# Kernel tuning notes

Measured on AMD Instinct MI355X. Metric: run time of the kernel, lower is better.

The kernel has to match this reference:

```python
import jax, jax.numpy as jnp
import numpy as np

D_MODEL = 2048
HEADS = 16
INNER = 8192
SEQ = 2048
BATCH = 1  # source code's mask.reshape(B,1,L,L) requires B==1
EPS = 1e-5


def _layer_norm(x, gamma, beta):
    mu = jnp.mean(x, axis=-1, keepdims=True)
    var = jnp.mean(jnp.square(x - mu), axis=-1, keepdims=True)
    return (x - mu) * jax.lax.rsqrt(var + EPS) * gamma + beta


def setup_inputs() -> dict:
    key = jax.random.key(0)
    ks = jax.random.split(key, 14)
    s = 0.02
    return {
        "x": jax.random.normal(ks[0], (BATCH, SEQ, D_MODEL), jnp.float32),
        # weights stored as (in, out)
        "Wqkv": jax.random.normal(ks[1], (D_MODEL, 3 * D_MODEL), jnp.float32) * s,
        "bqkv": jnp.zeros((3 * D_MODEL,), jnp.float32),
        "Wo": jax.random.normal(ks[2], (D_MODEL, D_MODEL), jnp.float32) * s,
        "bo": jnp.zeros((D_MODEL,), jnp.float32),
        "W1": jax.random.normal(ks[3], (D_MODEL, INNER), jnp.float32) * s,
        "b1": jnp.zeros((INNER,), jnp.float32),
        "W2": jax.random.normal(ks[4], (INNER, D_MODEL), jnp.float32) * s,
        "b2": jnp.zeros((D_MODEL,), jnp.float32),
        "g1": jnp.ones((D_MODEL,), jnp.float32),
        "be1": jnp.zeros((D_MODEL,), jnp.float32),
        "g2": jnp.ones((D_MODEL,), jnp.float32),
        "be2": jnp.zeros((D_MODEL,), jnp.float32),
    }


def reference(x, Wqkv, bqkv, Wo, bo, W1, b1, W2, b2, g1, be1, g2, be2):
    B, L, D = x.shape
    H, hd = HEADS, D // HEADS
    qkv = x @ Wqkv + bqkv                       # [B,L,3D]
    q, k, v = jnp.split(qkv, 3, axis=-1)
    q = q.reshape(B, L, H, hd)
    k = k.reshape(B, L, H, hd)
    v = v.reshape(B, L, H, hd)
    # NOTE: faithful to source, scale is 1/sqrt(D) not 1/sqrt(head_dim)
    scores = jnp.einsum("bqhd,bkhd->bhqk", q, k) / jnp.sqrt(jnp.float32(D))
    causal = jnp.tril(jnp.ones((L, L), bool))   # [L,L] broadcast over B,H
    scores = jnp.where(causal, scores, -jnp.inf)
    attn = jax.nn.softmax(scores, axis=-1)      # dropout = identity (eval)
    out = jnp.einsum("bhqk,bkhd->bqhd", attn, v).reshape(B, L, D)
    lin = out @ Wo + bo
    h = _layer_norm(x + lin, g1, be1)
    ff = jax.nn.gelu(h @ W1 + b1, approximate=False) @ W2 + b2
    return _layer_norm(h + ff, g2, be2)
```

## Files before the change

kernel.cpp:

```cpp
#include <hip/hip_runtime.h>
#include <hip/hip_bf16.h>

typedef unsigned short u16;
typedef __attribute__((ext_vector_type(8))) short frag8;
typedef __attribute__((ext_vector_type(4))) float facc4;

#define L_SEQ 2048
#define D_MODEL 2048
#define N_HEADS 16
#define HEAD_D 128
#define N_QKV 6144
#define D_INNER 8192

__device__ __forceinline__ u16 f2b(float f) {
    __hip_bfloat16 h = __float2bfloat16(f);
    return *reinterpret_cast<u16*>(&h);
}

__device__ __forceinline__ float b2f(u16 u) {
    __hip_bfloat16 h = *reinterpret_cast<__hip_bfloat16*>(&u);
    return __bfloat162float(h);
}

__device__ __forceinline__ void gload_lds16(const void* g, void* l) {
    __builtin_amdgcn_global_load_lds(
        (const __attribute__((address_space(1))) unsigned int*)g,
        (__attribute__((address_space(3))) unsigned int*)l, 16, 0, 0);
}

__device__ __forceinline__ float gelu_exact(float x) {
    return 0.5f * x * (1.0f + erff(x * 0.7071067811865475f));
}

__global__ __launch_bounds__(256) void cvt_bf16_kernel(const float* __restrict__ in, u16* __restrict__ out, int n) {
    const int i = (blockIdx.x * 256 + threadIdx.x) * 8;
    if (i >= n) return;
    float4 a = *(const float4*)(in + i);
    float4 b = *(const float4*)(in + i + 4);
    u16 tmp[8];
    tmp[0] = f2b(a.x); tmp[1] = f2b(a.y); tmp[2] = f2b(a.z); tmp[3] = f2b(a.w);
    tmp[4] = f2b(b.x); tmp[5] = f2b(b.y); tmp[6] = f2b(b.z); tmp[7] = f2b(b.w);
    *(uint4*)(out + i) = *(uint4*)tmp;
}

__global__ __launch_bounds__(256) void tr_cvt64(const float* __restrict__ in, u16* __restrict__ out, int R, int C) {
    __shared__ float t[64][68];
    const int bx = blockIdx.x * 64;
    const int by = blockIdx.y * 64;
    const int tid = threadIdx.x;
    {
        const int r = tid >> 2;
        const int c4 = (tid & 3) * 16;
        const float* src = in + (size_t)(by + r) * C + bx + c4;
#pragma unroll
        for (int j = 0; j < 4; ++j)
            *(float4*)&t[r][c4 + 4 * j] = *(const float4*)(src + 4 * j);
    }
    __syncthreads();
    {
        const int cc = tid >> 2;
        const int rr0 = (tid & 3) * 16;
        u16 tmp[16];
#pragma unroll
        for (int j = 0; j < 16; ++j) tmp[j] = f2b(t[rr0 + j][cc]);
        u16* dst = out + (size_t)(bx + cc) * R + by + rr0;
        *(uint4*)(dst) = *(uint4*)&tmp[0];
        *(uint4*)(dst + 8) = *(uint4*)&tmp[8];
    }
}

template <int EPI>
__global__ __launch_bounds__(512, 2) void gemm256(const u16* __restrict__ A, const u16* __restrict__ Bt,
                                                  const float* __restrict__ bias, void* __restrict__ Cout,
                                                  u16* __restrict__ q0, u16* __restrict__ q1,
                                                  u16* __restrict__ q2, u16* __restrict__ q3,
                                                  int M, int N, int K, int kseg, int nbm) {
    __shared__ u16 lds[2 * 32768];
    const int tid = threadIdx.x;
    const int lane = tid & 63, wid = tid >> 6;
    const int wm = wid >> 2, wn = wid & 3;
    const int l15 = lane & 15, g4 = lane >> 4;

    const int nwg = gridDim.x;
    const int q8 = nwg >> 3;
    const int wg = (blockIdx.x & 7) * q8 + (blockIdx.x >> 3);
    const int bm = wg % nbm, bn = wg / nbm;
    const int kb = blockIdx.z * kseg;
    const int ksz = (blockIdx.z == (int)gridDim.z - 1) ? (K - kb) : kseg;
    const int nt = ksz >> 6;

    const int rr = tid >> 3;
    const int kk8 = tid & 7;
    const int srcE = (kk8 ^ (rr & 7)) << 3;
    const u16* aS = A + (size_t)(bm * 256 + rr) * K + kb + srcE;
    const u16* bS = Bt + (size_t)(bn * 256 + ((rr >> 5) << 6) + (rr & 31)) * K + kb + srcE;
    const size_t r128 = (size_t)128 * K;
    const size_t r64 = (size_t)64 * K;
    const size_t c32 = (size_t)32 * K;

    auto stA = [&](int tt, int h) {
        u16* d = &lds[((tt & 1) << 15) + (h << 13)];
        const u16* g = aS + (size_t)tt * 64 + (h ? r64 : 0);
        gload_lds16(g, d + tid * 8);
        gload_lds16(g + r128, d + 4096 + tid * 8);
    };
    auto stB = [&](int tt, int h) {
        u16* d = &lds[((tt & 1) << 15) + 16384 + (h << 13)];
        const u16* g = bS + (size_t)tt * 64 + (h ? c32 : 0);
        gload_lds16(g, d + tid * 8);
        gload_lds16(g + r128, d + 4096 + tid * 8);
    };

    const int ch0 = (g4 ^ (l15 & 7)) << 3;
    const int ch1 = ch0 ^ 32;
    const int aRdBase = (wm * 64 + l15) * 64;
    const int bRdBase = (wn * 32 + l15) * 64;

    frag8 a[4][2], b0[2][2], b1[2][2];
    facc4 acc[8][4] = {};

    auto rdA = [&](int bufo, int mh) {
#pragma unroll
        for (int mi = 0; mi < 4; ++mi) {
            const int base = bufo + mh * 8192 + aRdBase + mi * 1024;
            a[mi][0] = *(const frag8*)&lds[base + ch0];
            a[mi][1] = *(const frag8*)&lds[base + ch1];
        }
    };
    auto rdB = [&](int bufo, int nh, frag8(&bb)[2][2]) {
#pragma unroll
        for (int ni = 0; ni < 2; ++ni) {
            const int base = bufo + 16384 + nh * 8192 + bRdBase + ni * 1024;
            bb[ni][0] = *(const frag8*)&lds[base + ch0];
            bb[ni][1] = *(const frag8*)&lds[base + ch1];
        }
    };
    auto quad = [&](int mh, int nh, frag8(&bb)[2][2]) {
        __builtin_amdgcn_s_setprio(1);
#pragma unroll
        for (int kh = 0; kh < 2; ++kh)
#pragma unroll
            for (int mi = 0; mi < 4; ++mi)
#pragma unroll
                for (int ni = 0; ni < 2; ++ni)
                    acc[mh * 4 + mi][nh * 2 + ni] =
                        __builtin_amdgcn_mfma_f32_16x16x32_bf16(a[mi][kh], bb[ni][kh],
                                                                acc[mh * 4 + mi][nh * 2 + ni], 0, 0, 0);
        __builtin_amdgcn_s_setprio(0);
    };

#define SB __builtin_amdgcn_sched_barrier(0)
#define BAR __builtin_amdgcn_s_barrier()

    stA(0, 0); stB(0, 0); stB(0, 1); stA(0, 1);
    if (nt > 1) { stA(1, 0); stB(1, 0); stB(1, 1); }
    if (nt > 2) asm volatile("s_waitcnt vmcnt(6)" ::: "memory");
    else        asm volatile("s_waitcnt vmcnt(0)" ::: "memory");
    BAR; SB;

    for (int t = 0; t < nt; ++t) {
        const int bufo = (t & 1) << 15;
        rdA(bufo, 0);
        rdB(bufo, 0, b0);
        if (t + 1 < nt) stA(t + 1, 1);
        SB; BAR; SB;
        quad(0, 0, b0);
        BAR; SB;
        rdB(bufo, 1, b1);
        if (t + 2 < nt) stA(t + 2, 0);
        SB; BAR; SB;
        quad(0, 1, b1);
        BAR; SB;
        rdA(bufo, 1);
        if (t + 2 < nt) stB(t + 2, 0);
        SB; BAR; SB;
        quad(1, 0, b0);
        BAR; SB;
        if (t + 2 < nt) stB(t + 2, 1);
        SB; BAR; SB;
        quad(1, 1, b1);
        if (t + 2 < nt) asm volatile("s_waitcnt vmcnt(6)" ::: "memory");
        else            asm volatile("s_waitcnt vmcnt(0)" ::: "memory");
        BAR; SB;
    }
#undef SB
#undef BAR

    const int row0 = bm * 256 + wm * 128 + g4 * 4;
    const int col0 = bn * 256 + wn * 64 + l15;
    u16* pout = nullptr;
    if (EPI == 3) {
        const int z = blockIdx.z;
        pout = (z == 0) ? q0 : (z == 1) ? q1 : (z == 2) ? q2 : q3;
    }
#pragma unroll
    for (int nf = 0; nf < 4; nf++) {
        const int col = col0 + nf * 16;
        const float bv = (EPI == 3) ? 0.0f : bias[col];
#pragma unroll
        for (int mf = 0; mf < 8; mf++) {
#pragma unroll
            for (int r = 0; r < 4; r++) {
                const int row = row0 + mf * 16 + r;
                float v = acc[mf][nf][r] + bv;
                if (EPI == 2) v = gelu_exact(v);
                if (EPI == 0)
                    ((float*)Cout)[(size_t)row * N + col] = v;
                else if (EPI == 3)
                    pout[(size_t)row * N + col] = f2b(v);
                else
                    ((u16*)Cout)[(size_t)row * N + col] = f2b(v);
            }
        }
    }
}

__global__ __launch_bounds__(256) void attn_kernel(const u16* __restrict__ qkv, u16* __restrict__ out) {
    __shared__ u16 kT[2][64 * 128];
    __shared__ u16 vT[2][128 * 64];
    const int h = blockIdx.y;
    const int qb = (blockIdx.y < 8) ? ((int)gridDim.x - 1 - (int)blockIdx.x) : (int)blockIdx.x;
    const int tid = threadIdx.x;
    const int lane = tid & 63, w = tid >> 6;
    const int l15 = lane & 15, g4 = lane >> 4;
    const int q0 = qb * 64 + w * 16;
    const float scale = 0.022097086912079608f;

    frag8 qf[4];
    {
        const u16* qrow = qkv + (size_t)(q0 + l15) * N_QKV + h * HEAD_D + g4 * 8;
#pragma unroll
        for (int c = 0; c < 4; c++) qf[c] = *(const frag8*)(qrow + c * 32);
    }

    float m_run = -1e30f, l_run = 0.0f;
    facc4 o[8] = {};

    const int src0 = ((g4 & 1) << 5) + l15;
    const int src1 = src0 + 16;
    const bool hi = (g4 & 2) != 0;

    const int nt = qb + 1;

    auto stageK = [&](int kbase, int buf) {
        const u16* kg_ptr = qkv + (size_t)kbase * N_QKV + D_MODEL + h * HEAD_D;
#pragma unroll
        for (int p = 0; p < 4; ++p) {
            const int c = p * 256 + tid;
            const int row = c >> 4;
            const int colb = (c & 15) << 4;
            const int srcb = colb ^ ((row & 7) << 4);
            gload_lds16(kg_ptr + (size_t)row * N_QKV + (srcb >> 1), &kT[buf][c * 8]);
        }
    };
    auto loadV = [&](int kbase, uint4 (&vv)[4]) {
        const u16* vg_ptr = qkv + (size_t)kbase * N_QKV + 2 * D_MODEL + h * HEAD_D;
#pragma unroll
        for (int i = 0; i < 4; ++i)
            vv[i] = *(const uint4*)(vg_ptr + (size_t)lane * N_QKV + w * 32 + i * 8);
    };
    auto writeV = [&](const uint4 (&vv)[4], int buf) {
#pragma unroll
        for (int i = 0; i < 4; ++i) {
            const u16* pv = (const u16*)&vv[i];
#pragma unroll
            for (int e = 0; e < 8; ++e) {
                const int d = w * 32 + i * 8 + e;
                vT[buf][d * 64 + ((((lane >> 3) ^ (d & 7)) << 3) | (lane & 7))] = pv[e];
            }
        }
    };

    {
        uint4 vv[4];
        stageK(0, 0);
        loadV(0, vv);
        writeV(vv, 0);
    }
    __syncthreads();

    for (int t = 0; t < nt; ++t) {
        const int buf = t & 1;
        const int kbase = t * 64;
        const bool last = (t == nt - 1);

        uint4 vv[4];
        if (!last) {
            stageK(kbase + 64, buf ^ 1);
            loadV(kbase + 64, vv);
        }

        const u16* kTb = kT[buf];
        const u16* vTb = vT[buf];
        float st[16];
        float mx = -1e30f;
#pragma unroll
        for (int ks = 0; ks < 4; ++ks) {
            const bool active = !last || (ks <= w);
            if (active) {
                facc4 s = {};
                const int kl = ks * 16 + l15;
#pragma unroll
                for (int c = 0; c < 4; ++c) {
                    const int colb = (g4 * 16 + c * 64) ^ ((kl & 7) << 4);
                    frag8 kf = *(const frag8*)&kTb[kl * 128 + (colb >> 1)];
                    s = __builtin_amdgcn_mfma_f32_16x16x32_bf16(kf, qf[c], s, 0, 0, 0);
                }
#pragma unroll
                for (int r = 0; r < 4; ++r) {
                    float v = s[r] * scale;
                    if (last) {
                        const int key = kbase + ks * 16 + g4 * 4 + r;
                        if (key > q0 + l15) v = -1e30f;
                    }
                    st[ks * 4 + r] = v;
                    mx = fmaxf(mx, v);
                }
            } else {
#pragma unroll
                for (int r = 0; r < 4; ++r) st[ks * 4 + r] = -1e30f;
            }
        }

        mx = fmaxf(mx, __shfl_xor(mx, 16));
        mx = fmaxf(mx, __shfl_xor(mx, 32));
        const bool skip = __all(mx <= m_run + 8.0f);
        const float m_new = skip ? m_run : fmaxf(m_run, mx);
        const float alpha = __expf(m_run - m_new);
        float ps = 0.0f;
        uint2 pb[4];
#pragma unroll
        for (int ks = 0; ks < 4; ++ks) {
            const float p0 = __expf(st[ks * 4 + 0] - m_new);
            const float p1 = __expf(st[ks * 4 + 1] - m_new);
            const float p2 = __expf(st[ks * 4 + 2] - m_new);
            const float p3 = __expf(st[ks * 4 + 3] - m_new);
            ps += (p0 + p1) + (p2 + p3);
            pb[ks].x = (unsigned)f2b(p0) | ((unsigned)f2b(p1) << 16);
            pb[ks].y = (unsigned)f2b(p2) | ((unsigned)f2b(p3) << 16);
        }
        ps += __shfl_xor(ps, 16);
        ps += __shfl_xor(ps, 32);
        l_run = l_run * alpha + ps;
        m_run = m_new;
        if (!skip) {
#pragma unroll
            for (int c8 = 0; c8 < 8; ++c8)
#pragma unroll
                for (int r = 0; r < 4; ++r) o[c8][r] *= alpha;
        }

#pragma unroll
        for (int kp = 0; kp < 2; ++kp) {
            const bool kp_active = !last || (kp == 0) || (w >= 2);
            if (kp_active) {
                const uint2 a = pb[2 * kp], b = pb[2 * kp + 1];
                const unsigned a0 = __shfl(a.x, src0), a1 = __shfl(a.y, src0);
                const unsigned a2 = __shfl(a.x, src1), a3 = __shfl(a.y, src1);
                const unsigned b0 = __shfl(b.x, src0), b1 = __shfl(b.y, src0);
                const unsigned b2 = __shfl(b.x, src1), b3 = __shfl(b.y, src1);
                union { unsigned u[4]; frag8 f; } pu;
                pu.u[0] = hi ? b0 : a0;
                pu.u[1] = hi ? b1 : a1;
                pu.u[2] = hi ? b2 : a2;
                pu.u[3] = hi ? b3 : a3;
                const frag8 pf = pu.f;
#pragma unroll
                for (int c8 = 0; c8 < 8; ++c8) {
                    const int d = c8 * 16 + l15;
                    const int ch = (((kp * 4 + g4) ^ (l15 & 7)) << 3);
                    frag8 vf = *(const frag8*)&vTb[d * 64 + ch];
                    o[c8] = __builtin_amdgcn_mfma_f32_16x16x32_bf16(vf, pf, o[c8], 0, 0, 0);
                }
            }
        }

        if (!last) writeV(vv, buf ^ 1);
        __syncthreads();
    }

    const float inv_l = 1.0f / l_run;
    u16* orow = out + (size_t)(q0 + l15) * D_MODEL + h * HEAD_D;
#pragma unroll
    for (int c8 = 0; c8 < 8; ++c8) {
        uint2 st2;
        st2.x = (unsigned)f2b(o[c8][0] * inv_l) | ((unsigned)f2b(o[c8][1] * inv_l) << 16);
        st2.y = (unsigned)f2b(o[c8][2] * inv_l) | ((unsigned)f2b(o[c8][3] * inv_l) << 16);
        *(uint2*)&orow[c8 * 16 + g4 * 4] = st2;
    }
}

__global__ __launch_bounds__(256) void ln1_part_kernel(const float* __restrict__ x,
                                                       const u16* __restrict__ p0, const u16* __restrict__ p1,
                                                       const u16* __restrict__ p2, const u16* __restrict__ p3,
                                                       const float* __restrict__ bias,
                                                       const float* __restrict__ gamma, const float* __restrict__ beta,
                                                       u16* __restrict__ outb) {
    __shared__ float red[8];
    const int row = blockIdx.x;
    const int tid = threadIdx.x;
    const size_t rb = (size_t)row * D_MODEL;
    float v[8];
    float s = 0.0f, s2 = 0.0f;
#pragma unroll
    for (int i = 0; i < 8; i++) {
        const int c = tid + i * 256;
        float xv = x[rb + c] + bias[c] +
                   b2f(p0[rb + c]) + b2f(p1[rb + c]) + b2f(p2[rb + c]) + b2f(p3[rb + c]);
        v[i] = xv;
        s += xv;
        s2 += xv * xv;
    }
#pragma unroll
    for (int off = 32; off; off >>= 1) {
        s += __shfl_xor(s, off);
        s2 += __shfl_xor(s2, off);
    }
    if ((tid & 63) == 0) { red[(tid >> 6) * 2] = s; red[(tid >> 6) * 2 + 1] = s2; }
    __syncthreads();
    s = red[0] + red[2] + red[4] + red[6];
    s2 = red[1] + red[3] + red[5] + red[7];
    const float mean = s * (1.0f / D_MODEL);
    const float var = s2 * (1.0f / D_MODEL) - mean * mean;
    const float rstd = rsqrtf(var + 1e-5f);
#pragma unroll
    for (int i = 0; i < 8; i++) {
        const int c = tid + i * 256;
        outb[rb + c] = f2b((v[i] - mean) * rstd * gamma[c] + beta[c]);
    }
}

__global__ __launch_bounds__(256) void ln_part_kernel(const u16* __restrict__ hb,
                                                      const u16* __restrict__ p0, const u16* __restrict__ p1,
                                                      const u16* __restrict__ p2, const u16* __restrict__ p3,
                                                      const float* __restrict__ bias,
                                                      const float* __restrict__ gamma, const float* __restrict__ beta,
                                                      float* __restrict__ outf) {
    __shared__ float red[8];
    const int row = blockIdx.x;
    const int tid = threadIdx.x;
    const size_t rb = (size_t)row * D_MODEL;
    float v[8];
    float s = 0.0f, s2 = 0.0f;
#pragma unroll
    for (int i = 0; i < 8; i++) {
        const int c = tid + i * 256;
        float x = b2f(hb[rb + c]) + bias[c] +
                  b2f(p0[rb + c]) + b2f(p1[rb + c]) + b2f(p2[rb + c]) + b2f(p3[rb + c]);
        v[i] = x;
        s += x;
        s2 += x * x;
    }
#pragma unroll
    for (int off = 32; off; off >>= 1) {
        s += __shfl_xor(s, off);
        s2 += __shfl_xor(s2, off);
    }
    if ((tid & 63) == 0) { red[(tid >> 6) * 2] = s; red[(tid >> 6) * 2 + 1] = s2; }
    __syncthreads();
    s = red[0] + red[2] + red[4] + red[6];
    s2 = red[1] + red[3] + red[5] + red[7];
    const float mean = s * (1.0f / D_MODEL);
    const float var = s2 * (1.0f / D_MODEL) - mean * mean;
    const float rstd = rsqrtf(var + 1e-5f);
#pragma unroll
    for (int i = 0; i < 8; i++) {
        const int c = tid + i * 256;
        outf[rb + c] = (v[i] - mean) * rstd * gamma[c] + beta[c];
    }
}

extern "C" void kernel_launch(void* const* d_in, const int* in_sizes, int n_in,
                              void* d_out, int out_size, void* d_ws, size_t ws_size,
                              hipStream_t stream) {
    const float* x    = (const float*)d_in[0];
    const float* Wqkv = (const float*)d_in[1];
    const float* bqkv = (const float*)d_in[2];
    const float* Wo   = (const float*)d_in[3];
    const float* bo   = (const float*)d_in[4];
    const float* W1   = (const float*)d_in[5];
    const float* b1   = (const float*)d_in[6];
    const float* W2   = (const float*)d_in[7];
    const float* b2   = (const float*)d_in[8];
    const float* g1   = (const float*)d_in[9];
    const float* be1  = (const float*)d_in[10];
    const float* g2   = (const float*)d_in[11];
    const float* be2  = (const float*)d_in[12];

    char* ws = (char*)d_ws;
    const size_t MB = 1024 * 1024;
    u16*  xb     = (u16*)(ws + 0);
    u16*  WqkvT  = (u16*)(ws + 8 * MB);
    u16*  qkv    = (u16*)(ws + 32 * MB);
    u16*  attn_o = (u16*)(ws + 56 * MB);
    u16*  WoT    = (u16*)(ws + 8 * MB);
    u16*  pp0    = (u16*)(ws + 16 * MB);
    u16*  pp1    = (u16*)(ws + 24 * MB);
    u16*  pp2    = (u16*)(ws + 32 * MB);
    u16*  pp3    = (u16*)(ws + 40 * MB);
    u16*  hb     = (u16*)(ws + 0);
    u16*  W1T    = (u16*)(ws + 8 * MB);
    u16*  f1     = (u16*)(ws + 40 * MB);
    u16*  W2T    = (u16*)(ws + 72 * MB);
    u16*  part0  = (u16*)(ws + 8 * MB);
    u16*  part1  = (u16*)(ws + 16 * MB);
    u16*  part2  = (u16*)(ws + 24 * MB);
    u16*  part3  = (u16*)(ws + 32 * MB);

    cvt_bf16_kernel<<<2048, 256, 0, stream>>>(x, xb, L_SEQ * D_MODEL);
    tr_cvt64<<<dim3(N_QKV / 64, D_MODEL / 64), 256, 0, stream>>>(Wqkv, WqkvT, D_MODEL, N_QKV);
    gemm256<1><<<dim3(192, 1, 1), 512, 0, stream>>>(xb, WqkvT, bqkv, qkv, nullptr, nullptr, nullptr, nullptr,
                                                    L_SEQ, N_QKV, D_MODEL, D_MODEL, 8);
    attn_kernel<<<dim3(L_SEQ / 64, N_HEADS), 256, 0, stream>>>(qkv, attn_o);
    tr_cvt64<<<dim3(D_MODEL / 64, D_MODEL / 64), 256, 0, stream>>>(Wo, WoT, D_MODEL, D_MODEL);
    gemm256<3><<<dim3(64, 1, 4), 512, 0, stream>>>(attn_o, WoT, nullptr, nullptr, pp0, pp1, pp2, pp3,
                                                   L_SEQ, D_MODEL, D_MODEL, 512, 8);
    ln1_part_kernel<<<L_SEQ, 256, 0, stream>>>(x, pp0, pp1, pp2, pp3, bo, g1, be1, hb);
    tr_cvt64<<<dim3(D_INNER / 64, D_MODEL / 64), 256, 0, stream>>>(W1, W1T, D_MODEL, D_INNER);
    gemm256<2><<<dim3(256, 1, 1), 512, 0, stream>>>(hb, W1T, b1, f1, nullptr, nullptr, nullptr, nullptr,
                                                    L_SEQ, D_INNER, D_MODEL, D_MODEL, 8);
    tr_cvt64<<<dim3(D_MODEL / 64, D_INNER / 64), 256, 0, stream>>>(W2, W2T, D_INNER, D_MODEL);
    gemm256<3><<<dim3(64, 1, 4), 512, 0, stream>>>(f1, W2T, nullptr, nullptr, part0, part1, part2, part3,
                                                   L_SEQ, D_MODEL, D_INNER, 2048, 8);
    ln_part_kernel<<<L_SEQ, 256, 0, stream>>>(hb, part0, part1, part2, part3, b2, g2, be2, (float*)d_out);
}
```

Measured before the change: 449.1 us.

## Split causal attention KV range across two blocks and merge partials

Attention now launches twice as many blocks, each covering half of a query block's key tiles, and writes unnormalized fp32 outputs plus per-row max and sum. A new combine kernel merges the two halves with log-sum-exp weights and writes bf16. The goal is better load balance and occupancy for long causal rows, which previously ran as single long-lived blocks. The cost is fp32 partial traffic, an extra kernel launch and per-tile causal masking checks.

```diff
diff --git a/kernel.cpp b/kernel.cpp
--- a/kernel.cpp
+++ b/kernel.cpp
@@ -215,17 +215,25 @@
     }
 }
 
-__global__ __launch_bounds__(256) void attn_kernel(const u16* __restrict__ qkv, u16* __restrict__ out) {
+__global__ __launch_bounds__(256) void attn_kernel(const u16* __restrict__ qkv,
+                                                   float* __restrict__ O0, float* __restrict__ O1,
+                                                   float* __restrict__ ml) {
     __shared__ u16 kT[2][64 * 128];
     __shared__ u16 vT[2][128 * 64];
     const int h = blockIdx.y;
-    const int qb = (blockIdx.y < 8) ? ((int)gridDim.x - 1 - (int)blockIdx.x) : (int)blockIdx.x;
+    const int z = blockIdx.z;
+    const int qb = (blockIdx.y < 8) ? 31 - (int)blockIdx.x : (int)blockIdx.x;
     const int tid = threadIdx.x;
     const int lane = tid & 63, w = tid >> 6;
     const int l15 = lane & 15, g4 = lane >> 4;
     const int q0 = qb * 64 + w * 16;
     const float scale = 0.022097086912079608f;
 
+    const int ntt = qb + 1;
+    const int hsp = (ntt + 1) >> 1;
+    const int t0 = z ? hsp : 0;
+    const int t1 = z ? ntt : hsp;
+
     frag8 qf[4];
     {
         const u16* qrow = qkv + (size_t)(q0 + l15) * N_QKV + h * HEAD_D + g4 * 8;
@@ -239,8 +247,6 @@
     const int src0 = ((g4 & 1) << 5) + l15;
     const int src1 = src0 + 16;
     const bool hi = (g4 & 2) != 0;
-
-    const int nt = qb + 1;
 
     auto stageK = [&](int kbase, int buf) {
         const u16* kg_ptr = qkv + (size_t)kbase * N_QKV + D_MODEL + h * HEAD_D;
@@ -271,18 +277,18 @@
         }
     };
 
-    {
+    if (t0 < t1) {
         uint4 vv[4];
-        stageK(0, 0);
-        loadV(0, vv);
+        stageK(t0 * 64, 0);
+        loadV(t0 * 64, vv);
         writeV(vv, 0);
     }
     __syncthreads();
 
-    for (int t = 0; t < nt; ++t) {
-        const int buf = t & 1;
+    for (int t = t0; t < t1; ++t) {
+        const int buf = (t - t0) & 1;
         const int kbase = t * 64;
-        const bool last = (t == nt - 1);
+        const bool last = (t == t1 - 1);
 
         uint4 vv[4];
         if (!last) {
@@ -290,103 +296,132 @@
             loadV(kbase + 64, vv);
         }
 
-        const u16* kTb = kT[buf];
-        const u16* vTb = vT[buf];
-        float st[16];
-        float mx = -1e30f;
-#pragma unroll
-        for (int ks = 0; ks < 4; ++ks) {
-            const bool active = !last || (ks <= w);
-            if (active) {
-                facc4 s = {};
-                const int kl = ks * 16 + l15;
-#pragma unroll
-                for (int c = 0; c < 4; ++c) {
-                    const int colb = (g4 * 16 + c * 64) ^ ((kl & 7) << 4);
-                    frag8 kf = *(const frag8*)&kTb[kl * 128 + (colb >> 1)];
-                    s = __builtin_amdgcn_mfma_f32_16x16x32_bf16(kf, qf[c], s, 0, 0, 0);
-                }
-#pragma unroll
-                for (int r = 0; r < 4; ++r) {
-                    float v = s[r] * scale;
-                    if (last) {
-                        const int key = kbase + ks * 16 + g4 * 4 + r;
+        if (kbase <= q0 + 15) {
+            const u16* kTb = kT[buf];
+            const u16* vTb = vT[buf];
+            float st[16];
+            float mx = -1e30f;
+#pragma unroll
+            for (int ks = 0; ks < 4; ++ks) {
+                const int k0 = kbase + ks * 16;
+                if (k0 <= q0 + 15) {
+                    facc4 s = {};
+                    const int kl = ks * 16 + l15;
+#pragma unroll
+                    for (int c = 0; c < 4; ++c) {
+                        const int colb = (g4 * 16 + c * 64) ^ ((kl & 7) << 4);
+                        frag8 kf = *(const frag8*)&kTb[kl * 128 + (colb >> 1)];
+                        s = __builtin_amdgcn_mfma_f32_16x16x32_bf16(kf, qf[c], s, 0, 0, 0);
+                    }
+#pragma unroll
+                    for (int r = 0; r < 4; ++r) {
+                        float v = s[r] * scale;
+                        const int key = k0 + g4 * 4 + r;
                         if (key > q0 + l15) v = -1e30f;
+                        st[ks * 4 + r] = v;
+                        mx = fmaxf(mx, v);
                     }
-                    st[ks * 4 + r] = v;
-                    mx = fmaxf(mx, v);
-                }
-            } else {
-#pragma unroll
-                for (int r = 0; r < 4; ++r) st[ks * 4 + r] = -1e30f;
-            }
-        }
-
-        mx = fmaxf(mx, __shfl_xor(mx, 16));
-        mx = fmaxf(mx, __shfl_xor(mx, 32));
-        const bool skip = __all(mx <= m_run + 8.0f);
-        const float m_new = skip ? m_run : fmaxf(m_run, mx);
-        const float alpha = __expf(m_run - m_new);
-        float ps = 0.0f;
-        uint2 pb[4];
-#pragma unroll
-        for (int ks = 0; ks < 4; ++ks) {
-            const float p0 = __expf(st[ks * 4 + 0] - m_new);
-            const float p1 = __expf(st[ks * 4 + 1] - m_new);
-            const float p2 = __expf(st[ks * 4 + 2] - m_new);
-            const float p3 = __expf(st[ks * 4 + 3] - m_new);
-            ps += (p0 + p1) + (p2 + p3);
-            pb[ks].x = (unsigned)f2b(p0) | ((unsigned)f2b(p1) << 16);
-            pb[ks].y = (unsigned)f2b(p2) | ((unsigned)f2b(p3) << 16);
-        }
-        ps += __shfl_xor(ps, 16);
-        ps += __shfl_xor(ps, 32);
-        l_run = l_run * alpha + ps;
-        m_run = m_new;
-        if (!skip) {
-#pragma unroll
-            for (int c8 = 0; c8 < 8; ++c8)
-#pragma unroll
-                for (int r = 0; r < 4; ++r) o[c8][r] *= alpha;
-        }
-
-#pragma unroll
-        for (int kp = 0; kp < 2; ++kp) {
-            const bool kp_active = !last || (kp == 0) || (w >= 2);
-            if (kp_active) {
-                const uint2 a = pb[2 * kp], b = pb[2 * kp + 1];
-                const unsigned a0 = __shfl(a.x, src0), a1 = __shfl(a.y, src0);
-                const unsigned a2 = __shfl(a.x, src1), a3 = __shfl(a.y, src1);
-                const unsigned b0 = __shfl(b.x, src0), b1 = __shfl(b.y, src0);
-                const unsigned b2 = __shfl(b.x, src1), b3 = __shfl(b.y, src1);
-                union { unsigned u[4]; frag8 f; } pu;
-                pu.u[0] = hi ? b0 : a0;
-                pu.u[1] = hi ? b1 : a1;
-                pu.u[2] = hi ? b2 : a2;
-                pu.u[3] = hi ? b3 : a3;
-                const frag8 pf = pu.f;
-#pragma unroll
-                for (int c8 = 0; c8 < 8; ++c8) {
-                    const int d = c8 * 16 + l15;
-                    const int ch = (((kp * 4 + g4) ^ (l15 & 7)) << 3);
-                    frag8 vf = *(const frag8*)&vTb[d * 64 + ch];
-                    o[c8] = __builtin_amdgcn_mfma_f32_16x16x32_bf16(vf, pf, o[c8], 0, 0, 0);
+                } else {
+#pragma unroll
+                    for (int r = 0; r < 4; ++r) st[ks * 4 + r] = -1e30f;
                 }
             }
+
+            mx = fmaxf(mx, __shfl_xor(mx, 16));
+            mx = fmaxf(mx, __shfl_xor(mx, 32));
+            const bool skip = __all(mx <= m_run + 8.0f);
+            const float m_new = skip ? m_run : fmaxf(m_run, mx);
+            const float alpha = __expf(m_run - m_new);
+            float ps = 0.0f;
+            uint2 pb[4];
+#pragma unroll
+            for (int ks = 0; ks < 4; ++ks) {
+                const float p0 = __expf(st[ks * 4 + 0] - m_new);
+                const float p1 = __expf(st[ks * 4 + 1] - m_new);
+                const float p2 = __expf(st[ks * 4 + 2] - m_new);
+                const float p3 = __expf(st[ks * 4 + 3] - m_new);
+                ps += (p0 + p1) + (p2 + p3);
+                pb[ks].x = (unsigned)f2b(p0) | ((unsigned)f2b(p1) << 16);
+                pb[ks].y = (unsigned)f2b(p2) | ((unsigned)f2b(p3) << 16);
+            }
+            ps += __shfl_xor(ps, 16);
+            ps += __shfl_xor(ps, 32);
+            l_run = l_run * alpha + ps;
+            m_run = m_new;
+            if (!skip) {
+#pragma unroll
+                for (int c8 = 0; c8 < 8; ++c8)
+#pragma unroll
+                    for (int r = 0; r < 4; ++r) o[c8][r] *= alpha;
+            }
+
+#pragma unroll
+            for (int kp = 0; kp < 2; ++kp) {
+                if (kbase + kp * 32 <= q0 + 15) {
+                    const uint2 a = pb[2 * kp], b = pb[2 * kp + 1];
+                    const unsigned a0 = __shfl(a.x, src0), a1 = __shfl(a.y, src0);
+                    const unsigned a2 = __shfl(a.x, src1), a3 = __shfl(a.y, src1);
+                    const unsigned b0 = __shfl(b.x, src0), b1 = __shfl(b.y, src0);
+                    const unsigned b2 = __shfl(b.x, src1), b3 = __shfl(b.y, src1);
+                    union { unsigned u[4]; frag8 f; } pu;
+                    pu.u[0] = hi ? b0 : a0;
+                    pu.u[1] = hi ? b1 : a1;
+                    pu.u[2] = hi ? b2 : a2;
+                    pu.u[3] = hi ? b3 : a3;
+                    const frag8 pf = pu.f;
+#pragma unroll
+                    for (int c8 = 0; c8 < 8; ++c8) {
+                        const int d = c8 * 16 + l15;
+                        const int ch = (((kp * 4 + g4) ^ (l15 & 7)) << 3);
+                        frag8 vf = *(const frag8*)&vTb[d * 64 + ch];
+                        o[c8] = __builtin_amdgcn_mfma_f32_16x16x32_bf16(vf, pf, o[c8], 0, 0, 0);
+                    }
+                }
+            }
         }
 
         if (!last) writeV(vv, buf ^ 1);
         __syncthreads();
     }
 
-    const float inv_l = 1.0f / l_run;
-    u16* orow = out + (size_t)(q0 + l15) * D_MODEL + h * HEAD_D;
-#pragma unroll
-    for (int c8 = 0; c8 < 8; ++c8) {
-        uint2 st2;
-        st2.x = (unsigned)f2b(o[c8][0] * inv_l) | ((unsigned)f2b(o[c8][1] * inv_l) << 16);
-        st2.y = (unsigned)f2b(o[c8][2] * inv_l) | ((unsigned)f2b(o[c8][3] * inv_l) << 16);
-        *(uint2*)&orow[c8 * 16 + g4 * 4] = st2;
+    const int row = q0 + l15;
+    if (g4 == 0) {
+        const size_t mlo = (((size_t)z * N_HEADS + h) * L_SEQ + row) * 2;
+        ml[mlo + 0] = m_run;
+        ml[mlo + 1] = l_run;
+    }
+    if (t0 < t1) {
+        float* Op = z ? O1 : O0;
+        float* orow = Op + (size_t)row * D_MODEL + h * HEAD_D;
+#pragma unroll
+        for (int c8 = 0; c8 < 8; ++c8)
+            *(facc4*)&orow[c8 * 16 + g4 * 4] = o[c8];
+    }
+}
+
+__global__ __launch_bounds__(256) void attn_combine(const float* __restrict__ O0, const float* __restrict__ O1,
+                                                    const float* __restrict__ ml, u16* __restrict__ out) {
+    const int row = blockIdx.x;
+    const int tid = threadIdx.x;
+    const size_t rb = (size_t)row * D_MODEL;
+#pragma unroll
+    for (int i = 0; i < 8; ++i) {
+        const int c = tid + i * 256;
+        const int h = c >> 7;
+        const size_t o0 = (((size_t)0 * N_HEADS + h) * L_SEQ + row) * 2;
+        const size_t o1 = (((size_t)1 * N_HEADS + h) * L_SEQ + row) * 2;
+        const float m0 = ml[o0 + 0], l0 = ml[o0 + 1];
+        const float m1 = ml[o1 + 0], l1 = ml[o1 + 1];
+        float v;
+        if (l1 > 0.0f) {
+            const float m = fmaxf(m0, m1);
+            const float w0 = __expf(m0 - m);
+            const float w1 = __expf(m1 - m);
+            v = (O0[rb + c] * w0 + O1[rb + c] * w1) / (l0 * w0 + l1 * w1);
+        } else {
+            v = O0[rb + c] / l0;
+        }
+        out[rb + c] = f2b(v);
     }
 }
 
@@ -492,7 +527,10 @@
     u16*  xb     = (u16*)(ws + 0);
     u16*  WqkvT  = (u16*)(ws + 8 * MB);
     u16*  qkv    = (u16*)(ws + 32 * MB);
-    u16*  attn_o = (u16*)(ws + 56 * MB);
+    float* O0    = (float*)(ws + 0);
+    float* O1    = (float*)(ws + 16 * MB);
+    float* mlbuf = (float*)(ws + 56 * MB);
+    u16*  attn_o = (u16*)(ws + 57 * MB);
     u16*  WoT    = (u16*)(ws + 8 * MB);
     u16*  pp0    = (u16*)(ws + 16 * MB);
     u16*  pp1    = (u16*)(ws + 24 * MB);
@@ -511,7 +549,8 @@
     tr_cvt64<<<dim3(N_QKV / 64, D_MODEL / 64), 256, 0, stream>>>(Wqkv, WqkvT, D_MODEL, N_QKV);
     gemm256<1><<<dim3(192, 1, 1), 512, 0, stream>>>(xb, WqkvT, bqkv, qkv, nullptr, nullptr, nullptr, nullptr,
                                                     L_SEQ, N_QKV, D_MODEL, D_MODEL, 8);
-    attn_kernel<<<dim3(L_SEQ / 64, N_HEADS), 256, 0, stream>>>(qkv, attn_o);
+    attn_kernel<<<dim3(L_SEQ / 64, N_HEADS, 2), 256, 0, stream>>>(qkv, O0, O1, mlbuf);
+    attn_combine<<<L_SEQ, 256, 0, stream>>>(O0, O1, mlbuf, attn_o);
     tr_cvt64<<<dim3(D_MODEL / 64, D_MODEL / 64), 256, 0, stream>>>(Wo, WoT, D_MODEL, D_MODEL);
     gemm256<3><<<dim3(64, 1, 4), 512, 0, stream>>>(attn_o, WoT, nullptr, nullptr, pp0, pp1, pp2, pp3,
                                                    L_SEQ, D_MODEL, D_MODEL, 512, 8);
```

After: 458.1 us. No clear change (+2.0%).
